# Kernel tuning notes

Measured on AMD Instinct MI355X. Metric: run time of the kernel, lower is better.

## Reference

```python
import jax, jax.numpy as jnp
import numpy as np

B, N, C = 4, 1024, 768          # batch, tokens, embed_dim
D, H, HD, FF = 12, 12, 64, 3072  # depth, heads, head_dim, mlp hidden
LN_EPS = 1e-5


def setup_inputs() -> dict:
    key = jax.random.key(0)
    ks = jax.random.split(key, 12)
    w = lambda i, shape: jax.random.normal(ks[i], shape, jnp.float32) * 0.02
    return {
        "x": jax.random.normal(ks[0], (B, N, C), jnp.float32),
        "pos_x": jax.random.normal(ks[1], (B, N, C), jnp.float32),
        # stacked per-layer params (leading dim D)
        "qkv_w": w(2, (D, 3 * C, C)), "qkv_b": w(3, (D, 3 * C)),
        "proj_w": w(4, (D, C, C)),    "proj_b": w(5, (D, C)),
        "fc1_w": w(6, (D, FF, C)),    "fc1_b": w(7, (D, FF)),
        "fc2_w": w(8, (D, C, FF)),    "fc2_b": w(9, (D, C)),
        "ln1_g": jnp.ones((D, C), jnp.float32), "ln1_b": jnp.zeros((D, C), jnp.float32),
        "ln2_g": jnp.ones((D, C), jnp.float32), "ln2_b": jnp.zeros((D, C), jnp.float32),
        "normf_g": jnp.ones((C,), jnp.float32), "normf_b": jnp.zeros((C,), jnp.float32),
    }


def _ln(x, g, b):
    mu = jnp.mean(x, axis=-1, keepdims=True)
    var = jnp.mean((x - mu) ** 2, axis=-1, keepdims=True)
    return (x - mu) * jax.lax.rsqrt(var + LN_EPS) * g + b


def reference(x, pos_x, qkv_w, qkv_b, proj_w, proj_b, fc1_w, fc1_b, fc2_w, fc2_b,
              ln1_g, ln1_b, ln2_g, ln2_b, normf_g, normf_b):
    scale = 1.0 / jnp.sqrt(jnp.float32(HD))
    x = x + pos_x  # pos added once (add_pos_at_every_layer=False)

    def block(xc, p):
        qw, qb, pw, pb, f1w, f1b, f2w, f2b, g1, b1, g2, b2 = p
        h = _ln(xc, g1, b1)
        qkv = jnp.einsum('bnc,oc->bno', h, qw) + qb            # [B,N,3C]
        qkv = qkv.reshape(B, N, 3, H, HD).transpose(2, 0, 3, 1, 4)
        q, k, v = qkv[0], qkv[1], qkv[2]                       # [B,H,N,HD]
        attn = jax.nn.softmax(jnp.einsum('bhnd,bhmd->bhnm', q, k) * scale, axis=-1)
        o = jnp.einsum('bhnm,bhmd->bhnd', attn, v)
        o = o.transpose(0, 2, 1, 3).reshape(B, N, C)
        xc = xc + (jnp.einsum('bnc,oc->bno', o, pw) + pb)      # residual + proj
        h2 = _ln(xc, g2, b2)
        hid = jax.nn.gelu(jnp.einsum('bnc,fc->bnf', h2, f1w) + f1b, approximate=False)
        ffn = jnp.einsum('bnf,of->bno', hid, f2w) + f2b
        xc = xc + ffn
        return xc, None

    xs = (qkv_w, qkv_b, proj_w, proj_b, fc1_w, fc1_b, fc2_w, fc2_b,
          ln1_g, ln1_b, ln2_g, ln2_b)
    x, _ = jax.lax.scan(block, x, xs)
    return _ln(x, normf_g, normf_b)  # postnorm
```

## Files before the change

kernel.cpp:

```cpp
#include <hip/hip_runtime.h>
#include <hip/hip_bf16.h>
#include <math.h>

typedef __bf16 bf16;
typedef __bf16 bf16x8 __attribute__((ext_vector_type(8)));
typedef __bf16 bf16x4 __attribute__((ext_vector_type(4)));
typedef float  f32x4  __attribute__((ext_vector_type(4)));

#define B_  4
#define N_  1024
#define C_  768
#define H_  12
#define HD_ 64
#define FF_ 3072
#define T_  (B_*N_)
#define D_  12

__device__ __forceinline__ void gld_lds16(const void* g, void* l) {
    __builtin_amdgcn_global_load_lds(
        (const __attribute__((address_space(1))) void*)g,
        (__attribute__((address_space(3))) void*)l, 16, 0, 0);
}

#define SEAL() do {                                         \
    asm volatile("s_waitcnt lgkmcnt(0)" ::: "memory");      \
    __builtin_amdgcn_sched_barrier(0);                      \
    __builtin_amdgcn_s_barrier();                           \
    __builtin_amdgcn_sched_barrier(0);                      \
} while (0)

__device__ __forceinline__ float gelu_f(float v) {
    const float ax = fabsf(v) * 0.70710678118f;
    const float t  = __frcp_rn(1.0f + 0.3275911f * ax);
    float p = 1.061405429f;
    p = p * t - 1.453152027f;
    p = p * t + 1.421413741f;
    p = p * t - 0.284496736f;
    p = p * t + 0.254829592f;
    const float e = p * t * __expf(-ax * ax);
    const float erfv = (v >= 0.f) ? (1.0f - e) : (e - 1.0f);
    return 0.5f * v * (1.0f + erfv);
}

template<typename WT, int MODE>
__global__ __launch_bounds__(256) void gemm_bt(
    const bf16* __restrict__ A, const WT* __restrict__ Bt,
    const float* __restrict__ bias, bf16* __restrict__ out,
    float* __restrict__ resid, int M, int N, int Kfull, int Ks)
{
    constexpr bool BF = (sizeof(WT) == 2);
    constexpr int NB  = BF ? 2 : 1;
    __shared__ __align__(16) bf16 lA[NB][64*64];
    __shared__ __align__(16) WT   lB[NB][128*64];
    const int tid  = threadIdx.x;
    const int lane = tid & 63, wave = tid >> 6;
    const int lo = lane & 15, hi = lane >> 4;
    const int wm = wave & 1, wn = wave >> 1;

    const int xcd = blockIdx.x & 7;
    const int w   = blockIdx.x >> 3;
    const int gy  = N >> 7;
    const int gz  = Kfull / Ks;
    const int gyz = gy * gz;
    const int bx  = (xcd & 3) * 16 + (w & 15);
    const int byz = (xcd >> 2) * (gyz >> 1) + (w >> 4);
    const int by  = byz % gy;
    const int bz  = byz / gy;
    const int row0 = bx * 64, col0 = by * 128;
    const int k0base = bz * Ks;
    const int nt = Ks >> 6;

    f32x4 acc[2][4];
#pragma unroll
    for (int i = 0; i < 2; i++)
#pragma unroll
        for (int j = 0; j < 4; j++) acc[i][j] = (f32x4){0.f, 0.f, 0.f, 0.f};

    if constexpr (BF) {
        const bf16* pA[2]; int wAo[2];
#pragma unroll
        for (int r = 0; r < 2; ++r) {
            const int c = tid + r * 256;
            const int rw = c >> 3, kc = c & 7;
            pA[r]  = A + (size_t)(row0 + rw) * Kfull + k0base + kc * 8;
            wAo[r] = rw * 64 + (kc ^ (rw & 7)) * 8;
        }
        const bf16* pB[4]; int wBo[4];
#pragma unroll
        for (int r = 0; r < 4; ++r) {
            const int c = tid + r * 256;
            const int rw = c >> 3, kc = c & 7;
            pB[r]  = (const bf16*)Bt + (size_t)(col0 + rw) * Kfull + k0base + kc * 8;
            wBo[r] = rw * 64 + (kc ^ (rw & 7)) * 8;
        }
        bf16x8 rA[2], rB[4];
        auto loadT = [&](int t) {
#pragma unroll
            for (int r = 0; r < 2; ++r) rA[r] = *(const bf16x8*)(pA[r] + t * 64);
#pragma unroll
            for (int r = 0; r < 4; ++r) rB[r] = *(const bf16x8*)(pB[r] + t * 64);
        };
        auto writeT = [&](int buf) {
#pragma unroll
            for (int r = 0; r < 2; ++r) *(bf16x8*)(&lA[buf][wAo[r]]) = rA[r];
#pragma unroll
            for (int r = 0; r < 4; ++r) *(bf16x8*)(&((bf16*)lB[buf])[wBo[r]]) = rB[r];
        };
        auto compute = [&](int buf) {
#pragma unroll 1
            for (int s = 0; s < 2; ++s) {
                bf16x8 af[2], bfr[4];
#pragma unroll
                for (int i = 0; i < 2; i++) {
                    const int rowA = wm * 32 + i * 16 + lo;
                    const int ca = (s * 4 + hi) ^ (lo & 7);
                    af[i] = *(const bf16x8*)(&lA[buf][rowA * 64 + ca * 8]);
                }
#pragma unroll
                for (int i = 0; i < 4; i++) {
                    const int rowB = wn * 64 + i * 16 + lo;
                    const int cc = (s * 4 + hi) ^ (lo & 7);
                    bfr[i] = *(const bf16x8*)(&((const bf16*)lB[buf])[rowB * 64 + cc * 8]);
                }
#pragma unroll
                for (int mi = 0; mi < 2; mi++)
#pragma unroll
                    for (int ni = 0; ni < 4; ni++)
                        acc[mi][ni] = __builtin_amdgcn_mfma_f32_16x16x32_bf16(
                            af[mi], bfr[ni], acc[mi][ni], 0, 0, 0);
            }
        };

        loadT(0);
        writeT(0);
        if (nt > 1) loadT(1);
        SEAL();
        int cur = 0;
#pragma unroll 1
        for (int t = 0; t < nt; ++t) {
            compute(cur);
            if (t + 1 < nt) {
                writeT(cur ^ 1);
                if (t + 2 < nt) loadT(t + 2);
            }
            SEAL();
            cur ^= 1;
        }
    } else {
        for (int t = 0; t < nt; ++t) {
#pragma unroll
            for (int r = 0; r < 2; ++r) {
                const int cb    = r * 256 + wave * 64;
                const int chunk = cb + lane;
                const int rw = chunk >> 3, kc = chunk & 7;
                const int kcs = kc ^ (rw & 7);
                gld_lds16(A + (size_t)(row0 + rw) * Kfull + k0base + t * 64 + kcs * 8,
                          lA[0] + cb * 8);
            }
#pragma unroll
            for (int r = 0; r < 8; ++r) {
                const int cb    = r * 256 + wave * 64;
                const int chunk = cb + lane;
                const int rw = chunk >> 4, kc = chunk & 15;
                const int kcs = kc ^ ((rw & 7) << 1);
                gld_lds16(Bt + (size_t)(col0 + rw) * Kfull + k0base + t * 64 + kcs * 4,
                          (float*)lB[0] + cb * 4);
            }
            __syncthreads();
#pragma unroll 1
            for (int s = 0; s < 2; ++s) {
                bf16x8 af[2], bfr[4];
#pragma unroll
                for (int i = 0; i < 2; i++) {
                    const int rowA = wm * 32 + i * 16 + lo;
                    const int ca = (s * 4 + hi) ^ (lo & 7);
                    af[i] = *(const bf16x8*)(&lA[0][rowA * 64 + ca * 8]);
                }
#pragma unroll
                for (int i = 0; i < 4; i++) {
                    const int rowB = wn * 64 + i * 16 + lo;
                    const float* base = (const float*)lB[0] + rowB * 64;
                    const int c0 = (s * 8 + hi * 2) ^ ((lo & 7) << 1);
                    const f32x4 u0 = *(const f32x4*)(base + c0 * 4);
                    const f32x4 u1 = *(const f32x4*)(base + (c0 + 1) * 4);
                    bf16x8 f;
#pragma unroll
                    for (int e = 0; e < 4; e++) { f[e] = (bf16)u0[e]; f[4+e] = (bf16)u1[e]; }
                    bfr[i] = f;
                }
#pragma unroll
                for (int mi = 0; mi < 2; mi++)
#pragma unroll
                    for (int ni = 0; ni < 4; ni++)
                        acc[mi][ni] = __builtin_amdgcn_mfma_f32_16x16x32_bf16(
                            af[mi], bfr[ni], acc[mi][ni], 0, 0, 0);
            }
            __syncthreads();
        }
    }

    const float bscale = (bz == 0) ? 1.0f : 0.0f;
#pragma unroll
    for (int mi = 0; mi < 2; mi++) {
#pragma unroll
        for (int ni = 0; ni < 4; ni++) {
            const int gcol = col0 + wn * 64 + ni * 16 + lo;
            const float bv = bias[gcol] * bscale;
#pragma unroll
            for (int r = 0; r < 4; r++) {
                const int grow = row0 + wm * 32 + mi * 16 + hi * 4 + r;
                float v = acc[mi][ni][r] + bv;
                if (MODE == 1) v = gelu_f(v);
                if (MODE == 2) {
                    atomicAdd(&resid[(size_t)grow * N + gcol], v);
                } else {
                    out[(size_t)grow * N + gcol] = (bf16)v;
                }
            }
        }
    }
}

__global__ __launch_bounds__(256) void cvt_k(
    const float* __restrict__ src, bf16* __restrict__ dst)
{
    const int i = (blockIdx.x * 256 + threadIdx.x) * 8;
    const f32x4 a = *(const f32x4*)(src + i);
    const f32x4 b = *(const f32x4*)(src + i + 4);
    bf16x8 o;
#pragma unroll
    for (int e = 0; e < 4; e++) { o[e] = (bf16)a[e]; o[4 + e] = (bf16)b[e]; }
    *(bf16x8*)(dst + i) = o;
}

template<typename OutT>
__global__ __launch_bounds__(256) void ln_k(
    const float* __restrict__ x, const float* __restrict__ g,
    const float* __restrict__ b, OutT* __restrict__ out)
{
    const int wave = threadIdx.x >> 6, lane = threadIdx.x & 63;
    const int t = blockIdx.x * 4 + wave;
    const float* row = x + (size_t)t * C_;
    f32x4 v[3];
    float s = 0.f, ss = 0.f;
#pragma unroll
    for (int j = 0; j < 3; j++) {
        v[j] = *(const f32x4*)(row + (j * 64 + lane) * 4);
#pragma unroll
        for (int e = 0; e < 4; e++) { s += v[j][e]; ss += v[j][e] * v[j][e]; }
    }
#pragma unroll
    for (int off = 32; off > 0; off >>= 1) {
        s  += __shfl_xor(s, off);
        ss += __shfl_xor(ss, off);
    }
    const float mu  = s * (1.f / 768.f);
    const float var = ss * (1.f / 768.f) - mu * mu;
    const float rs  = rsqrtf(var + 1e-5f);
    OutT* orow = out + (size_t)t * C_;
#pragma unroll
    for (int j = 0; j < 3; j++) {
        const f32x4 gv = *(const f32x4*)(g + (j * 64 + lane) * 4);
        const f32x4 bv = *(const f32x4*)(b + (j * 64 + lane) * 4);
#pragma unroll
        for (int e = 0; e < 4; e++)
            orow[(j * 64 + lane) * 4 + e] = (OutT)((v[j][e] - mu) * rs * gv[e] + bv[e]);
    }
}

__global__ __launch_bounds__(256) void addpos_k(
    const float* __restrict__ x, const float* __restrict__ p, float* __restrict__ o)
{
    const int i = (blockIdx.x * 256 + threadIdx.x) * 4;
    const f32x4 xv = *(const f32x4*)(x + i);
    const f32x4 pv = *(const f32x4*)(p + i);
    f32x4 ov;
#pragma unroll
    for (int e = 0; e < 4; e++) ov[e] = xv[e] + pv[e];
    *(f32x4*)(o + i) = ov;
}

#define SKD_ 72
#define SVK_ 136
#define SPK_ 136
__global__ __launch_bounds__(256) void attn_k(
    const bf16* __restrict__ qkv, bf16* __restrict__ out)
{
    const int id2 = (blockIdx.x & 7) * 96 + (blockIdx.x >> 3);
    const int qt = id2 & 15;
    const int bh = id2 >> 4;
    const int b = bh / H_, h = bh % H_;
    const int lane = threadIdx.x & 63, wave = threadIdx.x >> 6;
    const int lo = lane & 15, hi = lane >> 4;

    __shared__ __align__(16) bf16 lK[128 * SKD_];
    __shared__ __align__(16) bf16 lV[64 * SVK_];
    __shared__ __align__(16) bf16 lP[4][16 * SPK_];

    const size_t tokbase = (size_t)b * N_;

    const bf16* qptr = qkv + (tokbase + qt * 64 + wave * 16 + lo) * (3 * C_) + h * HD_;
    bf16x8 qf0 = *(const bf16x8*)(qptr + hi * 8);
    bf16x8 qf1 = *(const bf16x8*)(qptr + 32 + hi * 8);
#pragma unroll
    for (int e = 0; e < 8; e++) {
        qf0[e] = (bf16)((float)qf0[e] * 0.125f);
        qf1[e] = (bf16)((float)qf1[e] * 0.125f);
    }
    bf16x8 onesf;
#pragma unroll
    for (int e = 0; e < 8; e++) onesf[e] = (bf16)1.0f;

    float m_r[4], l_r[4];
    f32x4 oacc[4];
#pragma unroll
    for (int r = 0; r < 4; r++) { m_r[r] = -1e30f; l_r[r] = 0.f; }
#pragma unroll
    for (int di = 0; di < 4; di++) oacc[di] = (f32x4){0.f, 0.f, 0.f, 0.f};

    for (int kt = 0; kt < 8; ++kt) {
        const int kb0 = kt * 128;
#pragma unroll
        for (int r = 0; r < 4; ++r) {
            const int chunk = r * 256 + threadIdx.x;
            const int key = chunk >> 3, dc = chunk & 7;
            const bf16* kp = qkv + (tokbase + kb0 + key) * (3 * C_) + C_ + h * HD_ + dc * 8;
            *(bf16x8*)(lK + key * SKD_ + dc * 8) = *(const bf16x8*)kp;
        }
#pragma unroll
        for (int r = 0; r < 4; ++r) {
            const int chunk = r * 256 + threadIdx.x;
            const int d = chunk & 63, kg = chunk >> 6;
            const bf16* vp = qkv + (tokbase + kb0 + kg * 8) * (3 * C_)
                           + 2 * C_ + h * HD_ + d;
            bf16x8 tv;
#pragma unroll
            for (int i = 0; i < 8; i++) tv[i] = vp[(size_t)i * (3 * C_)];
            *(bf16x8*)(lV + d * SVK_ + kg * 8) = tv;
        }
        __syncthreads();

        f32x4 sacc[8];
#pragma unroll
        for (int kb = 0; kb < 8; kb++) {
            const bf16x8 b0 = *(const bf16x8*)(lK + (kb * 16 + lo) * SKD_ + hi * 8);
            const bf16x8 b1 = *(const bf16x8*)(lK + (kb * 16 + lo) * SKD_ + 32 + hi * 8);
            f32x4 a = (f32x4){0.f, 0.f, 0.f, 0.f};
            a = __builtin_amdgcn_mfma_f32_16x16x32_bf16(qf0, b0, a, 0, 0, 0);
            a = __builtin_amdgcn_mfma_f32_16x16x32_bf16(qf1, b1, a, 0, 0, 0);
            sacc[kb] = a;
        }

        float pm[4], mn[4];
#pragma unroll
        for (int r = 0; r < 4; r++) {
            float a0 = fmaxf(fmaxf(sacc[0][r], sacc[1][r]),
                             fmaxf(sacc[2][r], sacc[3][r]));
            float a1 = fmaxf(fmaxf(sacc[4][r], sacc[5][r]),
                             fmaxf(sacc[6][r], sacc[7][r]));
            pm[r] = fmaxf(a0, a1);
        }
        const int okd = (pm[0] <= m_r[0] + 8.f) && (pm[1] <= m_r[1] + 8.f)
                     && (pm[2] <= m_r[2] + 8.f) && (pm[3] <= m_r[3] + 8.f);
        const bool defer = __all(okd);
        if (defer) {
#pragma unroll
            for (int r = 0; r < 4; r++) mn[r] = m_r[r];
        } else {
#pragma unroll
            for (int r = 0; r < 4; r++) {
                float tm = pm[r];
#pragma unroll
                for (int off = 1; off < 16; off <<= 1)
                    tm = fmaxf(tm, __shfl_xor(tm, off));
                mn[r] = fmaxf(m_r[r], tm);
            }
        }
#pragma unroll
        for (int kb = 0; kb < 8; kb++)
#pragma unroll
            for (int r = 0; r < 4; r++) {
                const float p = __expf(sacc[kb][r] - mn[r]);
                lP[wave][(hi * 4 + r) * SPK_ + kb * 16 + lo] = (bf16)p;
            }

        bf16x8 pa[4];
#pragma unroll
        for (int s = 0; s < 4; s++)
            pa[s] = *(const bf16x8*)(&lP[wave][lo * SPK_ + s * 32 + hi * 8]);

        f32x4 ls = (f32x4){0.f, 0.f, 0.f, 0.f};
#pragma unroll
        for (int s = 0; s < 4; s++)
            ls = __builtin_amdgcn_mfma_f32_16x16x32_bf16(pa[s], onesf, ls, 0, 0, 0);

        if (defer) {
#pragma unroll
            for (int r = 0; r < 4; r++) l_r[r] += ls[r];
        } else {
            float alpha[4];
#pragma unroll
            for (int r = 0; r < 4; r++) {
                alpha[r] = __expf(m_r[r] - mn[r]);
                l_r[r] = l_r[r] * alpha[r] + ls[r];
                m_r[r] = mn[r];
            }
#pragma unroll
            for (int di = 0; di < 4; di++)
#pragma unroll
                for (int r = 0; r < 4; r++) oacc[di][r] *= alpha[r];
        }

#pragma unroll
        for (int di = 0; di < 4; di++) {
#pragma unroll
            for (int s = 0; s < 4; s++) {
                const bf16x8 v = *(const bf16x8*)(lV + (di * 16 + lo) * SVK_ + s * 32 + hi * 8);
                oacc[di] = __builtin_amdgcn_mfma_f32_16x16x32_bf16(pa[s], v, oacc[di], 0, 0, 0);
            }
        }
        __syncthreads();
    }

    float il[4];
#pragma unroll
    for (int r = 0; r < 4; r++) il[r] = 1.0f / l_r[r];
#pragma unroll
    for (int di = 0; di < 4; di++)
#pragma unroll
        for (int r = 0; r < 4; r++) {
            const size_t tok = tokbase + qt * 64 + wave * 16 + hi * 4 + r;
            out[tok * C_ + h * HD_ + di * 16 + lo] = (bf16)(oacc[di][r] * il[r]);
        }
}

extern "C" void kernel_launch(void* const* d_in, const int* in_sizes, int n_in,
                              void* d_out, int out_size, void* d_ws, size_t ws_size,
                              hipStream_t stream)
{
    const float* x      = (const float*)d_in[0];
    const float* pos_x  = (const float*)d_in[1];
    const float* qkv_w  = (const float*)d_in[2];
    const float* qkv_b  = (const float*)d_in[3];
    const float* proj_w = (const float*)d_in[4];
    const float* proj_b = (const float*)d_in[5];
    const float* fc1_w  = (const float*)d_in[6];
    const float* fc1_b  = (const float*)d_in[7];
    const float* fc2_w  = (const float*)d_in[8];
    const float* fc2_b  = (const float*)d_in[9];
    const float* ln1_g  = (const float*)d_in[10];
    const float* ln1_b  = (const float*)d_in[11];
    const float* ln2_g  = (const float*)d_in[12];
    const float* ln2_b  = (const float*)d_in[13];
    const float* nf_g   = (const float*)d_in[14];
    const float* nf_b   = (const float*)d_in[15];

    char* ws = (char*)d_ws;
    float* xres  = (float*)(ws);
    bf16* hbuf   = (bf16*)(ws + 12582912);
    bf16* qkvbuf = (bf16*)(ws + 18874368);
    bf16* attno  = (bf16*)(ws + 37748736);
    bf16* hid    = (bf16*)(ws + 44040192);
    bf16* wq     = (bf16*)(ws + 69206016);
    bf16* wp     = (bf16*)(ws + 111673344);
    bf16* w1     = (bf16*)(ws + 125829120);
    bf16* w2     = (bf16*)(ws + 182452224);
    const bool usebf16 = ws_size >= (size_t)239075328;

    addpos_k<<<T_ * C_ / 4 / 256, 256, 0, stream>>>(x, pos_x, xres);

    if (usebf16) {
        cvt_k<<<D_ * 3 * C_ * C_ / 2048, 256, 0, stream>>>(qkv_w, wq);
        cvt_k<<<D_ * C_ * C_ / 2048, 256, 0, stream>>>(proj_w, wp);
        cvt_k<<<D_ * FF_ * C_ / 2048, 256, 0, stream>>>(fc1_w, w1);
        cvt_k<<<D_ * C_ * FF_ / 2048, 256, 0, stream>>>(fc2_w, w2);
    }

    const int g_qkv  = (T_/64) * ((3*C_)/128);
    const int g_proj = (T_/64) * (C_/128) * 2;
    const int g_fc1  = (T_/64) * (FF_/128);
    const int g_fc2  = (T_/64) * (C_/128) * 2;

    for (int L = 0; L < D_; ++L) {
        ln_k<bf16><<<T_ / 4, 256, 0, stream>>>(xres, ln1_g + L * C_, ln1_b + L * C_, hbuf);
        if (usebf16) {
            gemm_bt<bf16,0><<<g_qkv, 256, 0, stream>>>(
                hbuf, wq + (size_t)L * 3 * C_ * C_, qkv_b + (size_t)L * 3 * C_,
                qkvbuf, nullptr, T_, 3 * C_, C_, C_);
        } else {
            gemm_bt<float,0><<<g_qkv, 256, 0, stream>>>(
                hbuf, qkv_w + (size_t)L * 3 * C_ * C_, qkv_b + (size_t)L * 3 * C_,
                qkvbuf, nullptr, T_, 3 * C_, C_, C_);
        }
        attn_k<<<N_ / 64 * B_ * H_, 256, 0, stream>>>(qkvbuf, attno);
        if (usebf16) {
            gemm_bt<bf16,2><<<g_proj, 256, 0, stream>>>(
                attno, wp + (size_t)L * C_ * C_, proj_b + (size_t)L * C_,
                nullptr, xres, T_, C_, C_, C_ / 2);
        } else {
            gemm_bt<float,2><<<g_proj, 256, 0, stream>>>(
                attno, proj_w + (size_t)L * C_ * C_, proj_b + (size_t)L * C_,
                nullptr, xres, T_, C_, C_, C_ / 2);
        }
        ln_k<bf16><<<T_ / 4, 256, 0, stream>>>(xres, ln2_g + L * C_, ln2_b + L * C_, hbuf);
        if (usebf16) {
            gemm_bt<bf16,1><<<g_fc1, 256, 0, stream>>>(
                hbuf, w1 + (size_t)L * FF_ * C_, fc1_b + (size_t)L * FF_,
                hid, nullptr, T_, FF_, C_, C_);
            gemm_bt<bf16,2><<<g_fc2, 256, 0, stream>>>(
                hid, w2 + (size_t)L * C_ * FF_, fc2_b + (size_t)L * C_,
                nullptr, xres, T_, C_, FF_, FF_ / 2);
        } else {
            gemm_bt<float,1><<<g_fc1, 256, 0, stream>>>(
                hbuf, fc1_w + (size_t)L * FF_ * C_, fc1_b + (size_t)L * FF_,
                hid, nullptr, T_, FF_, C_, C_);
            gemm_bt<float,2><<<g_fc2, 256, 0, stream>>>(
                hid, fc2_w + (size_t)L * C_ * FF_, fc2_b + (size_t)L * C_,
                nullptr, xres, T_, C_, FF_, FF_ / 2);
        }
    }
    ln_k<float><<<T_ / 4, 256, 0, stream>>>(xres, nf_g, nf_b, (float*)d_out);
}
```

Measured before the change: 2.410 ms.

## Enlarge GEMM tile to 128x128 with K-step 32 and split-K of 4

The GEMM block tile grows from 64x128 to 128x128, so each wave computes a 64x64 sub-tile (4x4 MFMAs). The K step per stage shrinks from 64 to 32, with a new XOR swizzle sized for 32-wide rows. The proj and fc2 split-K factor rises from 2 to 4 to keep the grid large. The goal is more operand reuse per LDS load and fewer blocks, at the cost of more accumulator registers (possibly lower occupancy) and more atomic traffic on the residual.

```diff
diff --git a/kernel.cpp b/kernel.cpp
--- a/kernel.cpp
+++ b/kernel.cpp
@@ -15,12 +15,6 @@
 #define FF_ 3072
 #define T_  (B_*N_)
 #define D_  12
-
-__device__ __forceinline__ void gld_lds16(const void* g, void* l) {
-    __builtin_amdgcn_global_load_lds(
-        (const __attribute__((address_space(1))) void*)g,
-        (__attribute__((address_space(3))) void*)l, 16, 0, 0);
-}
 
 #define SEAL() do {                                         \
     asm volatile("s_waitcnt lgkmcnt(0)" ::: "memory");      \
@@ -50,8 +44,8 @@
 {
     constexpr bool BF = (sizeof(WT) == 2);
     constexpr int NB  = BF ? 2 : 1;
-    __shared__ __align__(16) bf16 lA[NB][64*64];
-    __shared__ __align__(16) WT   lB[NB][128*64];
+    __shared__ __align__(16) bf16 lA[NB][128*32];
+    __shared__ __align__(16) WT   lB[NB][128*32];
     const int tid  = threadIdx.x;
     const int lane = tid & 63, wave = tid >> 6;
     const int lo = lane & 15, hi = lane >> 4;
@@ -62,73 +56,65 @@
     const int gy  = N >> 7;
     const int gz  = Kfull / Ks;
     const int gyz = gy * gz;
-    const int bx  = (xcd & 3) * 16 + (w & 15);
-    const int byz = (xcd >> 2) * (gyz >> 1) + (w >> 4);
+    const int bx  = (xcd & 3) * 8 + (w & 7);
+    const int byz = (xcd >> 2) * (gyz >> 1) + (w >> 3);
     const int by  = byz % gy;
     const int bz  = byz / gy;
-    const int row0 = bx * 64, col0 = by * 128;
+    const int row0 = bx * 128, col0 = by * 128;
     const int k0base = bz * Ks;
-    const int nt = Ks >> 6;
-
-    f32x4 acc[2][4];
-#pragma unroll
-    for (int i = 0; i < 2; i++)
+    const int nt = Ks >> 5;
+
+    f32x4 acc[4][4];
+#pragma unroll
+    for (int i = 0; i < 4; i++)
 #pragma unroll
         for (int j = 0; j < 4; j++) acc[i][j] = (f32x4){0.f, 0.f, 0.f, 0.f};
+
+    const int ca = (hi ^ ((lo >> 1) & 3)) * 8;
 
     if constexpr (BF) {
         const bf16* pA[2]; int wAo[2];
+        const bf16* pB[2]; int wBo[2];
 #pragma unroll
         for (int r = 0; r < 2; ++r) {
             const int c = tid + r * 256;
-            const int rw = c >> 3, kc = c & 7;
+            const int rw = c >> 2, kc = c & 3;
             pA[r]  = A + (size_t)(row0 + rw) * Kfull + k0base + kc * 8;
-            wAo[r] = rw * 64 + (kc ^ (rw & 7)) * 8;
-        }
-        const bf16* pB[4]; int wBo[4];
-#pragma unroll
-        for (int r = 0; r < 4; ++r) {
-            const int c = tid + r * 256;
-            const int rw = c >> 3, kc = c & 7;
+            wAo[r] = rw * 32 + (kc ^ ((rw >> 1) & 3)) * 8;
             pB[r]  = (const bf16*)Bt + (size_t)(col0 + rw) * Kfull + k0base + kc * 8;
-            wBo[r] = rw * 64 + (kc ^ (rw & 7)) * 8;
-        }
-        bf16x8 rA[2], rB[4];
+            wBo[r] = wAo[r];
+        }
+        bf16x8 rA[2], rB[2];
         auto loadT = [&](int t) {
 #pragma unroll
-            for (int r = 0; r < 2; ++r) rA[r] = *(const bf16x8*)(pA[r] + t * 64);
-#pragma unroll
-            for (int r = 0; r < 4; ++r) rB[r] = *(const bf16x8*)(pB[r] + t * 64);
+            for (int r = 0; r < 2; ++r) rA[r] = *(const bf16x8*)(pA[r] + t * 32);
+#pragma unroll
+            for (int r = 0; r < 2; ++r) rB[r] = *(const bf16x8*)(pB[r] + t * 32);
         };
         auto writeT = [&](int buf) {
 #pragma unroll
             for (int r = 0; r < 2; ++r) *(bf16x8*)(&lA[buf][wAo[r]]) = rA[r];
 #pragma unroll
-            for (int r = 0; r < 4; ++r) *(bf16x8*)(&((bf16*)lB[buf])[wBo[r]]) = rB[r];
+            for (int r = 0; r < 2; ++r) *(bf16x8*)(&((bf16*)lB[buf])[wBo[r]]) = rB[r];
         };
         auto compute = [&](int buf) {
-#pragma unroll 1
-            for (int s = 0; s < 2; ++s) {
-                bf16x8 af[2], bfr[4];
-#pragma unroll
-                for (int i = 0; i < 2; i++) {
-                    const int rowA = wm * 32 + i * 16 + lo;
-                    const int ca = (s * 4 + hi) ^ (lo & 7);
-                    af[i] = *(const bf16x8*)(&lA[buf][rowA * 64 + ca * 8]);
-                }
-#pragma unroll
-                for (int i = 0; i < 4; i++) {
-                    const int rowB = wn * 64 + i * 16 + lo;
-                    const int cc = (s * 4 + hi) ^ (lo & 7);
-                    bfr[i] = *(const bf16x8*)(&((const bf16*)lB[buf])[rowB * 64 + cc * 8]);
-                }
-#pragma unroll
-                for (int mi = 0; mi < 2; mi++)
-#pragma unroll
-                    for (int ni = 0; ni < 4; ni++)
-                        acc[mi][ni] = __builtin_amdgcn_mfma_f32_16x16x32_bf16(
-                            af[mi], bfr[ni], acc[mi][ni], 0, 0, 0);
-            }
+            bf16x8 af[4], bfr[4];
+#pragma unroll
+            for (int i = 0; i < 4; i++) {
+                const int rowA = wm * 64 + i * 16 + lo;
+                af[i] = *(const bf16x8*)(&lA[buf][rowA * 32 + ca]);
+            }
+#pragma unroll
+            for (int i = 0; i < 4; i++) {
+                const int rowB = wn * 64 + i * 16 + lo;
+                bfr[i] = *(const bf16x8*)(&((const bf16*)lB[buf])[rowB * 32 + ca]);
+            }
+#pragma unroll
+            for (int mi = 0; mi < 4; mi++)
+#pragma unroll
+                for (int ni = 0; ni < 4; ni++)
+                    acc[mi][ni] = __builtin_amdgcn_mfma_f32_16x16x32_bf16(
+                        af[mi], bfr[ni], acc[mi][ni], 0, 0, 0);
         };
 
         loadT(0);
@@ -142,73 +128,67 @@
             if (t + 1 < nt) {
                 writeT(cur ^ 1);
                 if (t + 2 < nt) loadT(t + 2);
-            }
-            SEAL();
+                SEAL();
+            }
             cur ^= 1;
         }
     } else {
         for (int t = 0; t < nt; ++t) {
 #pragma unroll
             for (int r = 0; r < 2; ++r) {
-                const int cb    = r * 256 + wave * 64;
-                const int chunk = cb + lane;
-                const int rw = chunk >> 3, kc = chunk & 7;
-                const int kcs = kc ^ (rw & 7);
-                gld_lds16(A + (size_t)(row0 + rw) * Kfull + k0base + t * 64 + kcs * 8,
-                          lA[0] + cb * 8);
-            }
-#pragma unroll
-            for (int r = 0; r < 8; ++r) {
-                const int cb    = r * 256 + wave * 64;
-                const int chunk = cb + lane;
-                const int rw = chunk >> 4, kc = chunk & 15;
-                const int kcs = kc ^ ((rw & 7) << 1);
-                gld_lds16(Bt + (size_t)(col0 + rw) * Kfull + k0base + t * 64 + kcs * 4,
-                          (float*)lB[0] + cb * 4);
+                const int c = tid + r * 256;
+                const int rw = c >> 2, kc = c & 3;
+                const bf16x8 v = *(const bf16x8*)(
+                    A + (size_t)(row0 + rw) * Kfull + k0base + t * 32 + kc * 8);
+                *(bf16x8*)(&lA[0][rw * 32 + (kc ^ ((rw >> 1) & 3)) * 8]) = v;
+            }
+#pragma unroll
+            for (int r = 0; r < 4; ++r) {
+                const int c = tid + r * 256;
+                const int rw = c >> 3, kc = c & 7;
+                const f32x4 v = *(const f32x4*)(
+                    (const float*)Bt + (size_t)(col0 + rw) * Kfull + k0base + t * 32 + kc * 4);
+                *(f32x4*)(&((float*)lB[0])[rw * 32 + (kc ^ (rw & 7)) * 4]) = v;
             }
             __syncthreads();
-#pragma unroll 1
-            for (int s = 0; s < 2; ++s) {
-                bf16x8 af[2], bfr[4];
-#pragma unroll
-                for (int i = 0; i < 2; i++) {
-                    const int rowA = wm * 32 + i * 16 + lo;
-                    const int ca = (s * 4 + hi) ^ (lo & 7);
-                    af[i] = *(const bf16x8*)(&lA[0][rowA * 64 + ca * 8]);
-                }
-#pragma unroll
-                for (int i = 0; i < 4; i++) {
-                    const int rowB = wn * 64 + i * 16 + lo;
-                    const float* base = (const float*)lB[0] + rowB * 64;
-                    const int c0 = (s * 8 + hi * 2) ^ ((lo & 7) << 1);
-                    const f32x4 u0 = *(const f32x4*)(base + c0 * 4);
-                    const f32x4 u1 = *(const f32x4*)(base + (c0 + 1) * 4);
-                    bf16x8 f;
-#pragma unroll
-                    for (int e = 0; e < 4; e++) { f[e] = (bf16)u0[e]; f[4+e] = (bf16)u1[e]; }
-                    bfr[i] = f;
-                }
-#pragma unroll
-                for (int mi = 0; mi < 2; mi++)
-#pragma unroll
-                    for (int ni = 0; ni < 4; ni++)
-                        acc[mi][ni] = __builtin_amdgcn_mfma_f32_16x16x32_bf16(
-                            af[mi], bfr[ni], acc[mi][ni], 0, 0, 0);
-            }
+            bf16x8 af[4], bfr[4];
+#pragma unroll
+            for (int i = 0; i < 4; i++) {
+                const int rowA = wm * 64 + i * 16 + lo;
+                af[i] = *(const bf16x8*)(&lA[0][rowA * 32 + ca]);
+            }
+#pragma unroll
+            for (int i = 0; i < 4; i++) {
+                const int rowB = wn * 64 + i * 16 + lo;
+                const float* base = (const float*)lB[0] + rowB * 32;
+                const int c0 = (2 * hi) ^ (lo & 7), c1 = (2 * hi + 1) ^ (lo & 7);
+                const f32x4 u0 = *(const f32x4*)(base + c0 * 4);
+                const f32x4 u1 = *(const f32x4*)(base + c1 * 4);
+                bf16x8 f;
+#pragma unroll
+                for (int e = 0; e < 4; e++) { f[e] = (bf16)u0[e]; f[4+e] = (bf16)u1[e]; }
+                bfr[i] = f;
+            }
+#pragma unroll
+            for (int mi = 0; mi < 4; mi++)
+#pragma unroll
+                for (int ni = 0; ni < 4; ni++)
+                    acc[mi][ni] = __builtin_amdgcn_mfma_f32_16x16x32_bf16(
+                        af[mi], bfr[ni], acc[mi][ni], 0, 0, 0);
             __syncthreads();
         }
     }
 
     const float bscale = (bz == 0) ? 1.0f : 0.0f;
 #pragma unroll
-    for (int mi = 0; mi < 2; mi++) {
+    for (int mi = 0; mi < 4; mi++) {
 #pragma unroll
         for (int ni = 0; ni < 4; ni++) {
             const int gcol = col0 + wn * 64 + ni * 16 + lo;
             const float bv = bias[gcol] * bscale;
 #pragma unroll
             for (int r = 0; r < 4; r++) {
-                const int grow = row0 + wm * 32 + mi * 16 + hi * 4 + r;
+                const int grow = row0 + wm * 64 + mi * 16 + hi * 4 + r;
                 float v = acc[mi][ni][r] + bv;
                 if (MODE == 1) v = gelu_f(v);
                 if (MODE == 2) {
@@ -476,10 +456,10 @@
         cvt_k<<<D_ * C_ * FF_ / 2048, 256, 0, stream>>>(fc2_w, w2);
     }
 
-    const int g_qkv  = (T_/64) * ((3*C_)/128);
-    const int g_proj = (T_/64) * (C_/128) * 2;
-    const int g_fc1  = (T_/64) * (FF_/128);
-    const int g_fc2  = (T_/64) * (C_/128) * 2;
+    const int g_qkv  = 32 * ((3*C_)/128);
+    const int g_proj = 32 * (C_/128) * 4;
+    const int g_fc1  = 32 * (FF_/128);
+    const int g_fc2  = 32 * (C_/128) * 4;
 
     for (int L = 0; L < D_; ++L) {
         ln_k<bf16><<<T_ / 4, 256, 0, stream>>>(xres, ln1_g + L * C_, ln1_b + L * C_, hbuf);
@@ -496,11 +476,11 @@
         if (usebf16) {
             gemm_bt<bf16,2><<<g_proj, 256, 0, stream>>>(
                 attno, wp + (size_t)L * C_ * C_, proj_b + (size_t)L * C_,
-                nullptr, xres, T_, C_, C_, C_ / 2);
+                nullptr, xres, T_, C_, C_, C_ / 4);
         } else {
             gemm_bt<float,2><<<g_proj, 256, 0, stream>>>(
                 attno, proj_w + (size_t)L * C_ * C_, proj_b + (size_t)L * C_,
-                nullptr, xres, T_, C_, C_, C_ / 2);
+                nullptr, xres, T_, C_, C_, C_ / 4);
         }
         ln_k<bf16><<<T_ / 4, 256, 0, stream>>>(xres, ln2_g + L * C_, ln2_b + L * C_, hbuf);
         if (usebf16) {
@@ -509,14 +489,14 @@
                 hid, nullptr, T_, FF_, C_, C_);
             gemm_bt<bf16,2><<<g_fc2, 256, 0, stream>>>(
                 hid, w2 + (size_t)L * C_ * FF_, fc2_b + (size_t)L * C_,
-                nullptr, xres, T_, C_, FF_, FF_ / 2);
+                nullptr, xres, T_, C_, FF_, FF_ / 4);
         } else {
             gemm_bt<float,1><<<g_fc1, 256, 0, stream>>>(
                 hbuf, fc1_w + (size_t)L * FF_ * C_, fc1_b + (size_t)L * FF_,
                 hid, nullptr, T_, FF_, C_, C_);
             gemm_bt<float,2><<<g_fc2, 256, 0, stream>>>(
                 hid, fc2_w + (size_t)L * C_ * FF_, fc2_b + (size_t)L * C_,
-                nullptr, xres, T_, C_, FF_, FF_ / 2);
+                nullptr, xres, T_, C_, FF_, FF_ / 4);
         }
     }
     ln_k<float><<<T_ / 4, 256, 0, stream>>>(xres, nf_g, nf_b, (float*)d_out);
```

Result: slower. 3.005 ms (+24.7%).
